# Performance work log

Hardware: AMD Instinct MI355X
Metric: run time of the kernel (lower is better)

The kernel has to match this reference:

```python
import jax, jax.numpy as jnp
import numpy as np

N = 8388608

def setup_inputs() -> dict:
    key = jax.random.key(0)
    k1, k2 = jax.random.split(key)
    preds = jax.random.normal(k1, (N, 5), dtype=jnp.float32)
    target = jax.random.normal(k2, (N, 3), dtype=jnp.float32)
    return {"preds": preds, "target": target}

def reference(preds, target):
    # main MSE over the first 3 quantile columns: [N, 3]
    main_mse = (preds[:, :3] - target[:, :3]) ** 2

    p2 = preds[:, 2]
    p3 = preds[:, 3]
    t2 = target[:, 2]

    # lower-range loss, vectorized form of the per-row if/elif/else: [N]
    lower = jnp.where(
        p3 > p2,
        jnp.float32(1000.0),
        jnp.where(p3 > t2 * 0.95, jnp.float32(0.0), (p3 - t2 * 0.95) ** 2),
    )

    # NOTE: the original code assigns upper_range_loss = torch.Tensor(lowe_range_loss),
    # i.e. the upper range loss is (buggily) a copy of the lower range loss.
    # We replicate that behavior faithfully.
    upper = lower

    # concatenate all loss elements (3N + N + N) and reduce with mean
    loss = jnp.concatenate([main_mse.ravel(), lower, upper])
    return jnp.mean(loss)
```

## Files before the change

### kernel.cpp

```cpp
#include <hip/hip_runtime.h>


#define NROWS 8388608
#define ROWS_PER_CHUNK 1024
#define NCHUNKS (NROWS / ROWS_PER_CHUNK)
#define PCHUNK (ROWS_PER_CHUNK * 5)
#define TCHUNK (ROWS_PER_CHUNK * 3)

__global__ void __launch_bounds__(256) qloss_partial(
    const float* __restrict__ preds,
    const float* __restrict__ target,
    double* __restrict__ ws)
{
    __shared__ float sp[PCHUNK];
    __shared__ float st[TCHUNK];

    const int t = threadIdx.x;
    double acc = 0.0;

    for (int chunk = blockIdx.x; chunk < NCHUNKS; chunk += gridDim.x) {
        const float4* gp = (const float4*)(preds + (size_t)chunk * PCHUNK);
        const float4* gt = (const float4*)(target + (size_t)chunk * TCHUNK);

        float4 rp[5], rt[3];
        #pragma unroll
        for (int k = 0; k < 5; ++k) rp[k] = gp[t + k * 256];
        #pragma unroll
        for (int k = 0; k < 3; ++k) rt[k] = gt[t + k * 256];
        #pragma unroll
        for (int k = 0; k < 5; ++k) ((float4*)sp)[t + k * 256] = rp[k];
        #pragma unroll
        for (int k = 0; k < 3; ++k) ((float4*)st)[t + k * 256] = rt[k];

        __syncthreads();

        float sum = 0.0f;
        #pragma unroll
        for (int rr = 0; rr < 4; ++rr) {
            const int r = t + rr * 256;
            const float p0 = sp[5*r + 0];
            const float p1 = sp[5*r + 1];
            const float p2 = sp[5*r + 2];
            const float p3 = sp[5*r + 3];
            const float t0 = st[3*r + 0];
            const float t1 = st[3*r + 1];
            const float t2 = st[3*r + 2];

            const float a0 = p0 - t0;
            const float a1 = p1 - t1;
            const float a2 = p2 - t2;
            const float m  = a0*a0 + a1*a1 + a2*a2;

            const float q = t2 * 0.95f;
            const float d = p3 - q;
            const float lower = (p3 > p2) ? 1000.0f : ((p3 > q) ? 0.0f : d * d);

            sum += m + 2.0f * lower;
        }
        acc += (double)sum;

        __syncthreads();
    }

    #pragma unroll
    for (int off = 32; off > 0; off >>= 1)
        acc += __shfl_down(acc, off, 64);

    __shared__ double red[4];
    const int lane = t & 63;
    const int wave = t >> 6;
    if (lane == 0) red[wave] = acc;
    __syncthreads();

    if (t == 0) {
        atomicAdd(ws, red[0] + red[1] + red[2] + red[3]);
    }
}

__global__ void qloss_final(const double* __restrict__ ws, float* __restrict__ out)
{
    *out = (float)(*ws / (5.0 * (double)NROWS));
}

extern "C" void kernel_launch(void* const* d_in, const int* in_sizes, int n_in,
                              void* d_out, int out_size, void* d_ws, size_t ws_size,
                              hipStream_t stream)
{
    const float* preds  = (const float*)d_in[0];
    const float* target = (const float*)d_in[1];
    float* out  = (float*)d_out;
    double* ws  = (double*)d_ws;

    hipMemsetAsync(ws, 0, sizeof(double), stream);

    qloss_partial<<<2048, 256, 0, stream>>>(preds, target, ws);
    qloss_final<<<1, 1, 0, stream>>>(ws, out);
}
```

Before: 296.8 us.

## Replace LDS-staged grid-stride loop with per-thread 8-row register loads

Each thread now loads 8 contiguous rows (40 pred floats, 24 target floats) directly into registers with nontemporal vector loads, removing the shared-memory staging, the barriers and the grid-stride loop. The grid grows to 4096 blocks so that each thread handles exactly one group. Per-thread contiguous loads leave lanes strided by 160 bytes, which costs access coalescing in exchange for dropping LDS traffic and synchronisation. The grid size is now hard-wired to the input size.

Result: slower. 371.0 us (+25.0%).

```diff
diff --git a/kernel.cpp b/kernel.cpp
--- a/kernel.cpp
+++ b/kernel.cpp
@@ -2,79 +2,69 @@
 
 
 #define NROWS 8388608
-#define ROWS_PER_CHUNK 1024
-#define NCHUNKS (NROWS / ROWS_PER_CHUNK)
-#define PCHUNK (ROWS_PER_CHUNK * 5)
-#define TCHUNK (ROWS_PER_CHUNK * 3)
+#define NGROUPS (NROWS / 4)
+#define BLOCK 256
+#define GRID 4096
+
+typedef float v4f __attribute__((ext_vector_type(4)));
 
 __global__ void __launch_bounds__(256) qloss_partial(
     const float* __restrict__ preds,
     const float* __restrict__ target,
     double* __restrict__ ws)
 {
-    __shared__ float sp[PCHUNK];
-    __shared__ float st[TCHUNK];
+    const int gid = blockIdx.x * BLOCK + threadIdx.x;
 
-    const int t = threadIdx.x;
+    const v4f* gp = (const v4f*)(preds + (size_t)gid * 40);
+    const v4f* gt = (const v4f*)(target + (size_t)gid * 24);
+
+    v4f p[10], t[6];
+    #pragma unroll
+    for (int k = 0; k < 10; ++k) p[k] = __builtin_nontemporal_load(gp + k);
+    #pragma unroll
+    for (int k = 0; k < 6; ++k)  t[k] = __builtin_nontemporal_load(gt + k);
+
+    const float* pf = (const float*)p;
+    const float* tf = (const float*)t;
+
     double acc = 0.0;
+    float sum = 0.0f;
+    #pragma unroll
+    for (int r = 0; r < 8; ++r) {
+        const float p0 = pf[5*r + 0];
+        const float p1 = pf[5*r + 1];
+        const float p2 = pf[5*r + 2];
+        const float p3 = pf[5*r + 3];
+        const float t0 = tf[3*r + 0];
+        const float t1 = tf[3*r + 1];
+        const float t2 = tf[3*r + 2];
 
-    for (int chunk = blockIdx.x; chunk < NCHUNKS; chunk += gridDim.x) {
-        const float4* gp = (const float4*)(preds + (size_t)chunk * PCHUNK);
-        const float4* gt = (const float4*)(target + (size_t)chunk * TCHUNK);
+        const float a0 = p0 - t0;
+        const float a1 = p1 - t1;
+        const float a2 = p2 - t2;
+        const float m  = a0*a0 + a1*a1 + a2*a2;
 
-        float4 rp[5], rt[3];
-        #pragma unroll
-        for (int k = 0; k < 5; ++k) rp[k] = gp[t + k * 256];
-        #pragma unroll
-        for (int k = 0; k < 3; ++k) rt[k] = gt[t + k * 256];
-        #pragma unroll
-        for (int k = 0; k < 5; ++k) ((float4*)sp)[t + k * 256] = rp[k];
-        #pragma unroll
-        for (int k = 0; k < 3; ++k) ((float4*)st)[t + k * 256] = rt[k];
+        const float q = t2 * 0.95f;
+        const float d = p3 - q;
+        const float lower = (p3 > p2) ? 1000.0f : ((p3 > q) ? 0.0f : d * d);
 
-        __syncthreads();
-
-        float sum = 0.0f;
-        #pragma unroll
-        for (int rr = 0; rr < 4; ++rr) {
-            const int r = t + rr * 256;
-            const float p0 = sp[5*r + 0];
-            const float p1 = sp[5*r + 1];
-            const float p2 = sp[5*r + 2];
-            const float p3 = sp[5*r + 3];
-            const float t0 = st[3*r + 0];
-            const float t1 = st[3*r + 1];
-            const float t2 = st[3*r + 2];
-
-            const float a0 = p0 - t0;
-            const float a1 = p1 - t1;
-            const float a2 = p2 - t2;
-            const float m  = a0*a0 + a1*a1 + a2*a2;
-
-            const float q = t2 * 0.95f;
-            const float d = p3 - q;
-            const float lower = (p3 > p2) ? 1000.0f : ((p3 > q) ? 0.0f : d * d);
-
-            sum += m + 2.0f * lower;
-        }
-        acc += (double)sum;
-
-        __syncthreads();
+        sum += m + 2.0f * lower;
+        if (r == 3) { acc += (double)sum; sum = 0.0f; }
     }
+    acc += (double)sum;
 
     #pragma unroll
     for (int off = 32; off > 0; off >>= 1)
         acc += __shfl_down(acc, off, 64);
 
     __shared__ double red[4];
-    const int lane = t & 63;
-    const int wave = t >> 6;
+    const int lane = threadIdx.x & 63;
+    const int wave = threadIdx.x >> 6;
     if (lane == 0) red[wave] = acc;
     __syncthreads();
 
-    if (t == 0) {
+    if (threadIdx.x == 0)
         atomicAdd(ws, red[0] + red[1] + red[2] + red[3]);
-    }
 }
 
 __global__ void qloss_final(const double* __restrict__ ws, float* __restrict__ out)
@@ -93,6 +83,6 @@
 
     hipMemsetAsync(ws, 0, sizeof(double), stream);
 
-    qloss_partial<<<2048, 256, 0, stream>>>(preds, target, ws);
+    qloss_partial<<<GRID, BLOCK, 0, stream>>>(preds, target, ws);
     qloss_final<<<1, 1, 0, stream>>>(ws, out);
 }
```
